# Performance work log

Measured on AMD Instinct MI355X. Metric: run time of the kernel, lower is better.

## Reference

```python
import jax, jax.numpy as jnp
import numpy as np

H = 8  # n_heads


def _accumulate(carry, args):
    # carry: csum [B,H,l,d], norm [B,H,l], prev_mx [B,H,l]  (l=L//H, d=D//H)
    csum, norm, prev_mx = carry
    Qs_t, K_t, V_t, c_mx = args
    revert = jnp.exp(prev_mx - c_mx)               # rescale old accum to new max
    add = jnp.exp(K_t - c_mx)                      # exp(k_t) stabilized
    norm = norm * revert + add                     # [B,H,l]
    csum = csum * revert[..., None] + add[..., None] * V_t[:, :, None, :]  # [B,H,l,d]
    y = jnp.einsum('bhl,bhld->bhd', Qs_t / norm, csum)
    return (csum, norm, c_mx), y


def setup_inputs() -> dict:
    key = jax.random.key(0)
    B, T, D, L = 4, 2048, 1024, 512
    k0, k1, k2, k3, k4 = jax.random.split(key, 5)
    X = jax.random.normal(k0, (B, T, D), jnp.float32)
    # lecun_normal: std = 1/sqrt(fan_in)
    Wk = jax.random.normal(k1, (D, L), jnp.float32) * (1.0 / np.sqrt(D))
    Wq = jax.random.normal(k2, (D, L), jnp.float32) * (1.0 / np.sqrt(D))
    Wv = jax.random.normal(k3, (D, D), jnp.float32) * (1.0 / np.sqrt(D))
    o_proj = jax.random.normal(k4, (D, D), jnp.float32) * (1.0 / np.sqrt(D))
    return {"X": X, "Wk": Wk, "Wq": Wq, "Wv": Wv, "o_proj": o_proj, "train": False}


def reference(X, Wk, Wq, Wv, o_proj, train):
    # train=False -> dropouts are deterministic identities
    B, T, D = X.shape
    L = Wk.shape[1]
    V = jnp.einsum('dm,btd->tbm', Wv, X).reshape(T, B, H, D // H)
    Q = jnp.einsum('dl,btd->tbl', Wq, X).reshape(T, B, H, L // H)
    K = jnp.einsum('dl,btd->tbl', Wk, X).reshape(T, B, H, L // H)
    maxi = jax.lax.stop_gradient(jax.lax.cummax(K, axis=0))  # running max over time
    Qs = jax.nn.softmax(Q, axis=-1)
    init = (jnp.zeros((B, H, L // H, D // H), X.dtype),
            jnp.zeros((B, H, L // H), X.dtype),
            K[0])
    _, y = jax.lax.scan(_accumulate, init, (Qs, K, V, maxi), unroll=8)
    y = y.transpose(1, 0, 2, 3).reshape(B, T, D)
    return y @ o_proj
```

## Files before the change

### kernel.cpp

```cpp
#include <hip/hip_runtime.h>
#include <hip/hip_bf16.h>


typedef __attribute__((ext_vector_type(8))) short bf16x8;
typedef __attribute__((ext_vector_type(4))) float f32x4;

__device__ inline ushort f2bf(float f) {
    unsigned u = __float_as_uint(f);
    unsigned r = (u + 0x7fff + ((u >> 16) & 1)) >> 16;
    return (ushort)r;
}
__device__ inline float bf2f(ushort h) { return __uint_as_float(((unsigned)h) << 16); }

__device__ inline void gload_lds16(const ushort* g, ushort* l) {
    __builtin_amdgcn_global_load_lds((const __attribute__((address_space(1))) void*)g,
                                     (__attribute__((address_space(3))) void*)l, 16, 0, 0);
}

__global__ __launch_bounds__(256) void prep_inputs_kernel(const float* __restrict__ X,
                                                          const float* __restrict__ Wq,
                                                          const float* __restrict__ Wk,
                                                          const float* __restrict__ Wv,
                                                          const float* __restrict__ Wo,
                                                          ushort* __restrict__ Xb,
                                                          ushort* __restrict__ WqkT,
                                                          ushort* __restrict__ WvT,
                                                          ushort* __restrict__ WoT) {
    if (blockIdx.x < 8192) {
        int i = blockIdx.x * 1024 + threadIdx.x * 4;
        float4 v = *(const float4*)(X + i);
        ushort4 o = {f2bf(v.x), f2bf(v.y), f2bf(v.z), f2bf(v.w)};
        *(ushort4*)(Xb + i) = o;
        return;
    }
    __shared__ float s[32][33];
    int t = blockIdx.x - 8192;
    const float* W; ushort* WT; int N, tile, rowoff;
    if (t < 512)       { W = Wq; WT = WqkT; N = 512;  tile = t;        rowoff = 0; }
    else if (t < 1024) { W = Wk; WT = WqkT; N = 512;  tile = t - 512;  rowoff = 512; }
    else if (t < 2048) { W = Wv; WT = WvT;  N = 1024; tile = t - 1024; rowoff = 0; }
    else               { W = Wo; WT = WoT;  N = 1024; tile = t - 2048; rowoff = 0; }
    int tilesX = N >> 5;
    int n0 = (tile % tilesX) * 32, k0 = (tile / tilesX) * 32;
    int tx = threadIdx.x & 31, ty0 = threadIdx.x >> 5;
#pragma unroll
    for (int r = 0; r < 4; ++r) {
        int row = ty0 + r * 8;
        s[row][tx] = W[(size_t)(k0 + row) * N + n0 + tx];
    }
    __syncthreads();
#pragma unroll
    for (int r = 0; r < 4; ++r) {
        int row = ty0 + r * 8;
        WT[(size_t)(rowoff + n0 + row) * 1024 + k0 + tx] = f2bf(s[tx][row]);
    }
}

__global__ __launch_bounds__(256) void qk_gemm(const ushort* __restrict__ A,
                                               const ushort* __restrict__ BT,
                                               ushort* __restrict__ Qb,
                                               ushort* __restrict__ Kbp,
                                               float* __restrict__ mbuf,
                                               float* __restrict__ sbuf) {
    __shared__ __align__(16) ushort As[128 * 32];
    __shared__ __align__(16) ushort Bs[128 * 32];
    __shared__ float sredM[2][128];
    __shared__ float sredS[2][128];
    const int K = 1024;
    const int tid = threadIdx.x;
    const int w = tid >> 6, lane = tid & 63;
    const int quad = lane >> 4, l15 = lane & 15;
    const int m0 = blockIdx.y * 128, n0 = blockIdx.x * 128;
    const int wm = (w & 1) * 64, wn = (w >> 1) * 64;
    f32x4 acc[4][4] = {};
    const int r0 = tid >> 2, kc = (tid & 3) * 8;
    const int r1 = 64 + r0;
    const ushort* Arow0 = A + (size_t)(m0 + r0) * K + kc;
    const ushort* Arow1 = A + (size_t)(m0 + r1) * K + kc;
    const ushort* Brow0 = BT + (size_t)(n0 + r0) * K + kc;
    const ushort* Brow1 = BT + (size_t)(n0 + r1) * K + kc;
    ushort* AsW0 = As + (w * 64) * 8;
    ushort* AsW1 = As + (256 + w * 64) * 8;
    ushort* BsW0 = Bs + (w * 64) * 8;
    ushort* BsW1 = Bs + (256 + w * 64) * 8;
    const ushort* afp = As + (wm + l15) * 32 + quad * 8;
    const ushort* bfp = Bs + (wn + l15) * 32 + quad * 8;
    for (int k0 = 0; k0 < K; k0 += 32) {
        gload_lds16(Arow0 + k0, AsW0);
        gload_lds16(Arow1 + k0, AsW1);
        gload_lds16(Brow0 + k0, BsW0);
        gload_lds16(Brow1 + k0, BsW1);
        __syncthreads();
        bf16x8 af[4], bf[4];
#pragma unroll
        for (int i = 0; i < 4; ++i) {
            af[i] = *(const bf16x8*)(afp + i * 16 * 32);
            bf[i] = *(const bf16x8*)(bfp + i * 16 * 32);
        }
#pragma unroll
        for (int i = 0; i < 4; ++i)
#pragma unroll
            for (int j = 0; j < 4; ++j)
                acc[i][j] = __builtin_amdgcn_mfma_f32_16x16x32_bf16(af[i], bf[j], acc[i][j], 0, 0, 0);
        __syncthreads();
    }
    const int crow = m0 + wm + quad * 4;
    const int ccol = n0 + wn + l15;
    if (n0 < 512) {
#pragma unroll
        for (int i = 0; i < 4; ++i)
#pragma unroll
            for (int r = 0; r < 4; ++r) {
                float x0 = acc[i][0][r], x1 = acc[i][1][r];
                float x2 = acc[i][2][r], x3 = acc[i][3][r];
                float m = fmaxf(fmaxf(x0, x1), fmaxf(x2, x3));
#pragma unroll
                for (int off = 1; off < 16; off <<= 1) m = fmaxf(m, __shfl_xor(m, off));
                float e0 = __expf(x0 - m), e1 = __expf(x1 - m);
                float e2 = __expf(x2 - m), e3 = __expf(x3 - m);
                float s = (e0 + e1) + (e2 + e3);
#pragma unroll
                for (int off = 1; off < 16; off <<= 1) s += __shfl_xor(s, off);
                float rs = 1.0f / s;
                acc[i][0][r] = e0 * rs; acc[i][1][r] = e1 * rs;
                acc[i][2][r] = e2 * rs; acc[i][3][r] = e3 * rs;
            }
#pragma unroll
        for (int i = 0; i < 4; ++i)
#pragma unroll
            for (int j = 0; j < 4; ++j) {
                f32x4 v = acc[i][j];
#pragma unroll
                for (int r = 0; r < 4; ++r)
                    Qb[(size_t)(crow + i * 16 + r) * 512 + ccol + j * 16] = f2bf(v[r]);
            }
    } else {
        int b = blockIdx.y >> 4, c = blockIdx.y & 15;
        float mj[4];
#pragma unroll
        for (int j = 0; j < 4; ++j) {
            float m = -1e30f;
#pragma unroll
            for (int i = 0; i < 4; ++i)
#pragma unroll
                for (int r = 0; r < 4; ++r) m = fmaxf(m, acc[i][j][r]);
            m = fmaxf(m, __shfl_xor(m, 16));
            m = fmaxf(m, __shfl_xor(m, 32));
            mj[j] = m;
        }
        if (quad == 0)
#pragma unroll
            for (int j = 0; j < 4; ++j) sredM[w & 1][(w >> 1) * 64 + j * 16 + l15] = mj[j];
        __syncthreads();
#pragma unroll
        for (int j = 0; j < 4; ++j) {
            int ci = (w >> 1) * 64 + j * 16 + l15;
            float M = fmaxf(sredM[0][ci], sredM[1][ci]);
            float s = 0.f;
#pragma unroll
            for (int i = 0; i < 4; ++i)
#pragma unroll
                for (int r = 0; r < 4; ++r) s += __expf(acc[i][j][r] - M);
            s += __shfl_xor(s, 16);
            s += __shfl_xor(s, 32);
            mj[j] = s;
        }
        if (quad == 0)
#pragma unroll
            for (int j = 0; j < 4; ++j) sredS[w & 1][(w >> 1) * 64 + j * 16 + l15] = mj[j];
        __syncthreads();
        if (tid < 128) {
            int Kcol = (n0 - 512) + tid;
            int h = Kcol >> 6, l = Kcol & 63;
            int idx = (((b * 8 + h) * 16 + c)) * 64 + l;
            mbuf[idx] = fmaxf(sredM[0][tid], sredM[1][tid]);
            sbuf[idx] = sredS[0][tid] + sredS[1][tid];
        }
#pragma unroll
        for (int i = 0; i < 4; ++i)
#pragma unroll
            for (int j = 0; j < 4; ++j) {
                f32x4 v = acc[i][j];
#pragma unroll
                for (int r = 0; r < 4; ++r)
                    Kbp[(size_t)(crow + i * 16 + r) * 512 + (ccol - 512) + j * 16] = f2bf(v[r]);
            }
    }
}

__global__ __launch_bounds__(256) void vt_gemm(const ushort* __restrict__ A,
                                               const ushort* __restrict__ BT,
                                               ushort* __restrict__ VT) {
    __shared__ __align__(16) ushort As[128 * 32];
    __shared__ __align__(16) ushort Bs[128 * 32];
    __shared__ __align__(16) ushort Ts[128 * 136];
    const int K = 1024;
    const int tid = threadIdx.x;
    const int w = tid >> 6, lane = tid & 63;
    const int quad = lane >> 4, l15 = lane & 15;
    const int m0 = blockIdx.y * 128, n0 = blockIdx.x * 128;
    const int wm = (w & 1) * 64, wn = (w >> 1) * 64;
    f32x4 acc[4][4] = {};
    const int r0 = tid >> 2, kc = (tid & 3) * 8;
    const int r1 = 64 + r0;
    const ushort* Arow0 = A + (size_t)(m0 + r0) * K + kc;
    const ushort* Arow1 = A + (size_t)(m0 + r1) * K + kc;
    const ushort* Brow0 = BT + (size_t)(n0 + r0) * K + kc;
    const ushort* Brow1 = BT + (size_t)(n0 + r1) * K + kc;
    ushort* AsW0 = As + (w * 64) * 8;
    ushort* AsW1 = As + (256 + w * 64) * 8;
    ushort* BsW0 = Bs + (w * 64) * 8;
    ushort* BsW1 = Bs + (256 + w * 64) * 8;
    const ushort* afp = As + (wm + l15) * 32 + quad * 8;
    const ushort* bfp = Bs + (wn + l15) * 32 + quad * 8;
    for (int k0 = 0; k0 < K; k0 += 32) {
        gload_lds16(Arow0 + k0, AsW0);
        gload_lds16(Arow1 + k0, AsW1);
        gload_lds16(Brow0 + k0, BsW0);
        gload_lds16(Brow1 + k0, BsW1);
        __syncthreads();
        bf16x8 af[4], bf[4];
#pragma unroll
        for (int i = 0; i < 4; ++i) {
            af[i] = *(const bf16x8*)(afp + i * 16 * 32);
            bf[i] = *(const bf16x8*)(bfp + i * 16 * 32);
        }
#pragma unroll
        for (int i = 0; i < 4; ++i)
#pragma unroll
            for (int j = 0; j < 4; ++j)
                acc[i][j] = __builtin_amdgcn_mfma_f32_16x16x32_bf16(af[i], bf[j], acc[i][j], 0, 0, 0);
        __syncthreads();
    }
#pragma unroll
    for (int i = 0; i < 4; ++i)
#pragma unroll
        for (int j = 0; j < 4; ++j) {
            f32x4 v = acc[i][j];
            int d = wn + j * 16 + l15;
            int t = wm + i * 16 + quad * 4;
            ushort4 o = {f2bf(v[0]), f2bf(v[1]), f2bf(v[2]), f2bf(v[3])};
            *(ushort4*)(Ts + d * 136 + t) = o;
        }
    __syncthreads();
    int b = m0 >> 11, tloc = m0 & 2047, h = n0 >> 7;
    ushort* base = VT + ((size_t)(b * 8 + h) * 128) * 2048 + tloc;
    int kk = tid & 7;
#pragma unroll
    for (int p = 0; p < 4; ++p) {
        int dd = p * 32 + (tid >> 3);
        const uint4* src = (const uint4*)(Ts + dd * 136 + kk * 16);
        uint4* dst = (uint4*)(base + (size_t)dd * 2048 + kk * 16);
        dst[0] = src[0];
        dst[1] = src[1];
    }
}

__global__ __launch_bounds__(256) void prep_scanP_kernel(const ushort* __restrict__ Kbuf,
                                                         const ushort* __restrict__ Qs,
                                                         const float* __restrict__ mbuf,
                                                         const float* __restrict__ sbuf,
                                                         ushort* __restrict__ abuf,
                                                         ushort* __restrict__ aTbuf,
                                                         ushort* __restrict__ Pbuf) {
    __shared__ float red[4][64];
    int blk = blockIdx.x, bh = blk >> 4, c = blk & 15;
    int b = bh >> 3, h = bh & 7;
    int tg = threadIdx.x >> 6, l = threadIdx.x & 63;
    float mc[16];
#pragma unroll
    for (int cc = 0; cc < 16; ++cc) mc[cc] = mbuf[(bh * 16 + cc) * 64 + l];
    float M = -1e30f;
#pragma unroll
    for (int cc = 0; cc < 16; ++cc) M = fmaxf(M, mc[cc]);
    float A0 = 0.f;
    for (int cc = 0; cc < c; ++cc) A0 += sbuf[(bh * 16 + cc) * 64 + l] * __expf(mc[cc] - M);
    const ushort* kp = Kbuf + ((size_t)(b * 2048 + c * 128 + tg * 32)) * 512 + h * 64 + l;
    const ushort* qp = Qs + ((size_t)(b * 2048 + c * 128 + tg * 32)) * 512 + h * 64 + l;
    float a[32];
#pragma unroll
    for (int i = 0; i < 32; ++i) a[i] = __expf(bf2f(kp[(size_t)i * 512]) - M);
    float part = 0.f;
#pragma unroll
    for (int i = 0; i < 32; ++i) part += a[i];
    red[tg][l] = part;
    __syncthreads();
    float A = A0;
    for (int g = 0; g < 4; ++g) {
        float v = red[g][l];
        A += (g < tg) ? v : 0.f;
    }
    ushort* ap = abuf + ((size_t)(bh * 2048 + c * 128 + tg * 32)) * 64 + l;
    ushort* pp = Pbuf + ((size_t)(bh * 2048 + c * 128 + tg * 32)) * 64 + l;
    ushort atmp[32];
#pragma unroll
    for (int i = 0; i < 32; ++i) {
        A += a[i];
        ushort ab16 = f2bf(a[i]);
        ap[(size_t)i * 64] = ab16;
        atmp[i] = ab16;
        pp[(size_t)i * 64] = f2bf(bf2f(qp[(size_t)i * 512]) / A);
    }
    ushort* atp = aTbuf + ((size_t)bh * 64 + l) * 2048 + c * 128 + tg * 32;
#pragma unroll
    for (int v = 0; v < 4; ++v) *(uint4*)(atp + v * 8) = *(const uint4*)(atmp + v * 8);
}

__global__ __launch_bounds__(256) void chunk_sums_mfma(const ushort* __restrict__ aT,
                                                       const ushort* __restrict__ VT,
                                                       float* __restrict__ S) {
    int blk = blockIdx.x, bh = blk >> 4, c = blk & 15;
    int w = threadIdx.x >> 6, lane = threadIdx.x & 63;
    int quad = lane >> 4, l15 = lane & 15;
    const ushort* vtb = VT + (size_t)bh * 128 * 2048 + c * 128;
    const ushort* atb = aT + (size_t)bh * 64 * 2048 + c * 128;
    f32x4 acc[2][4] = {};
#pragma unroll
    for (int ks = 0; ks < 4; ++ks) {
        bf16x8 af[2];
#pragma unroll
        for (int mi = 0; mi < 2; ++mi)
            af[mi] = *(const bf16x8*)(vtb + (size_t)(w * 32 + mi * 16 + l15) * 2048 + ks * 32 + quad * 8);
#pragma unroll
        for (int nj = 0; nj < 4; ++nj) {
            bf16x8 bfr = *(const bf16x8*)(atb + (size_t)(nj * 16 + l15) * 2048 + ks * 32 + quad * 8);
#pragma unroll
            for (int mi = 0; mi < 2; ++mi)
                acc[mi][nj] = __builtin_amdgcn_mfma_f32_16x16x32_bf16(af[mi], bfr, acc[mi][nj], 0, 0, 0);
        }
    }
    float* sp = S + (size_t)blk * 8192;
#pragma unroll
    for (int mi = 0; mi < 2; ++mi)
#pragma unroll
        for (int nj = 0; nj < 4; ++nj) {
            f32x4 v = acc[mi][nj];
#pragma unroll
            for (int r = 0; r < 4; ++r)
                sp[(w * 32 + mi * 16 + quad * 4 + r) * 64 + nj * 16 + l15] = v[r];
        }
}

__global__ __launch_bounds__(256) void chunk_prefix_kernel(float* __restrict__ Sbuf) {
    int gid = blockIdx.x * 256 + threadIdx.x;
    int l = gid & 63, d = (gid >> 6) & 127, bh = gid >> 13;
    float run = 0.f;
    for (int c = 0; c < 16; ++c) {
        size_t idx = (size_t)(bh * 16 + c) * 8192 + d * 64 + l;
        float t = Sbuf[idx];
        Sbuf[idx] = run;
        run += t;
    }
}

__global__ __launch_bounds__(256) void chunk_out_mfma(const ushort* __restrict__ ab,
                                                      const ushort* __restrict__ Pb,
                                                      const ushort* __restrict__ VT,
                                                      const float* __restrict__ S,
                                                      ushort* __restrict__ Yb) {
    __shared__ __align__(16) ushort Gs[128 * 136];
    int blk = blockIdx.x, bh = blk >> 4, c = blk & 15;
    int b = bh >> 3, h = bh & 7;
    int w = threadIdx.x >> 6, lane = threadIdx.x & 63;
    int quad = lane >> 4, l15 = lane & 15;
    const ushort* Pc = Pb + (size_t)(bh * 2048 + c * 128) * 64;
    const ushort* Ac = ab + (size_t)(bh * 2048 + c * 128) * 64;
    f32x4 g[8][2] = {};
#pragma unroll
    for (int ks = 0; ks < 2; ++ks) {
        bf16x8 bfr[2];
#pragma unroll
        for (int ni = 0; ni < 2; ++ni)
            bfr[ni] = *(const bf16x8*)(Pc + (w * 32 + ni * 16 + l15) * 64 + ks * 32 + quad * 8);
#pragma unroll
        for (int ms = 0; ms < 8; ++ms) {
            bf16x8 af = *(const bf16x8*)(Ac + (ms * 16 + l15) * 64 + ks * 32 + quad * 8);
#pragma unroll
            for (int ni = 0; ni < 2; ++ni)
                g[ms][ni] = __builtin_amdgcn_mfma_f32_16x16x32_bf16(af, bfr[ni], g[ms][ni], 0, 0, 0);
        }
    }
#pragma unroll
    for (int ms = 0; ms < 8; ++ms)
#pragma unroll
        for (int ni = 0; ni < 2; ++ni) {
            int iL = w * 32 + ni * 16 + l15;
            int sBase = ms * 16 + quad * 4;
            f32x4 v = g[ms][ni];
            ushort4 o;
            o.x = (sBase + 0 <= iL) ? f2bf(v[0]) : (ushort)0;
            o.y = (sBase + 1 <= iL) ? f2bf(v[1]) : (ushort)0;
            o.z = (sBase + 2 <= iL) ? f2bf(v[2]) : (ushort)0;
            o.w = (sBase + 3 <= iL) ? f2bf(v[3]) : (ushort)0;
            *(ushort4*)(Gs + iL * 136 + sBase) = o;
        }
    __syncthreads();
    const ushort* vtb = VT + (size_t)bh * 128 * 2048 + c * 128;
    const float* sp = S + (size_t)blk * 8192;
    f32x4 y[2][8] = {};
#pragma unroll
    for (int ks = 0; ks < 4; ++ks) {
        bf16x8 af[2];
#pragma unroll
        for (int mi = 0; mi < 2; ++mi)
            af[mi] = *(const bf16x8*)(Gs + (w * 32 + mi * 16 + l15) * 136 + ks * 32 + quad * 8);
#pragma unroll
        for (int nj = 0; nj < 8; ++nj) {
            bf16x8 bfr = *(const bf16x8*)(vtb + (size_t)(nj * 16 + l15) * 2048 + ks * 32 + quad * 8);
#pragma unroll
            for (int mi = 0; mi < 2; ++mi)
                y[mi][nj] = __builtin_amdgcn_mfma_f32_16x16x32_bf16(af[mi], bfr, y[mi][nj], 0, 0, 0);
        }
    }
#pragma unroll
    for (int ks = 0; ks < 2; ++ks) {
        bf16x8 af[2];
#pragma unroll
        for (int mi = 0; mi < 2; ++mi)
            af[mi] = *(const bf16x8*)(Pc + (w * 32 + mi * 16 + l15) * 64 + ks * 32 + quad * 8);
#pragma unroll
        for (int nj = 0; nj < 8; ++nj) {
            const float* s8 = sp + (nj * 16 + l15) * 64 + ks * 32 + quad * 8;
            float4 f0 = *(const float4*)s8;
            float4 f1 = *(const float4*)(s8 + 4);
            bf16x8 bfr;
            bfr[0] = (short)f2bf(f0.x); bfr[1] = (short)f2bf(f0.y);
            bfr[2] = (short)f2bf(f0.z); bfr[3] = (short)f2bf(f0.w);
            bfr[4] = (short)f2bf(f1.x); bfr[5] = (short)f2bf(f1.y);
            bfr[6] = (short)f2bf(f1.z); bfr[7] = (short)f2bf(f1.w);
#pragma unroll
            for (int mi = 0; mi < 2; ++mi)
                y[mi][nj] = __builtin_amdgcn_mfma_f32_16x16x32_bf16(af[mi], bfr, y[mi][nj], 0, 0, 0);
        }
    }
    ushort* yout = Yb + ((size_t)(b * 2048 + c * 128)) * 1024 + h * 128;
#pragma unroll
    for (int mi = 0; mi < 2; ++mi)
#pragma unroll
        for (int nj = 0; nj < 8; ++nj) {
            f32x4 v = y[mi][nj];
#pragma unroll
            for (int r = 0; r < 4; ++r) {
                int iL = w * 32 + mi * 16 + quad * 4 + r;
                yout[(size_t)iL * 1024 + nj * 16 + l15] = f2bf(v[r]);
            }
        }
}

__global__ __launch_bounds__(256) void mfma_gemm(const ushort* __restrict__ A,
                                                 const ushort* __restrict__ BT,
                                                 float* __restrict__ Cf,
                                                 int M, int N, int K) {
    __shared__ __align__(16) ushort As[128 * 32];
    __shared__ __align__(16) ushort Bs[128 * 32];
    const int tid = threadIdx.x;
    const int w = tid >> 6, lane = tid & 63;
    const int quad = lane >> 4, l15 = lane & 15;
    const int m0 = blockIdx.y * 128, n0 = blockIdx.x * 128;
    const int wm = (w & 1) * 64, wn = (w >> 1) * 64;
    f32x4 acc[4][4] = {};
    const int r0 = tid >> 2, kc = (tid & 3) * 8;
    const int r1 = 64 + r0;
    const ushort* Arow0 = A + (size_t)(m0 + r0) * K + kc;
    const ushort* Arow1 = A + (size_t)(m0 + r1) * K + kc;
    const ushort* Brow0 = BT + (size_t)(n0 + r0) * K + kc;
    const ushort* Brow1 = BT + (size_t)(n0 + r1) * K + kc;
    ushort* AsW0 = As + (w * 64) * 8;
    ushort* AsW1 = As + (256 + w * 64) * 8;
    ushort* BsW0 = Bs + (w * 64) * 8;
    ushort* BsW1 = Bs + (256 + w * 64) * 8;
    const ushort* afp = As + (wm + l15) * 32 + quad * 8;
    const ushort* bfp = Bs + (wn + l15) * 32 + quad * 8;
    for (int k0 = 0; k0 < K; k0 += 32) {
        gload_lds16(Arow0 + k0, AsW0);
        gload_lds16(Arow1 + k0, AsW1);
        gload_lds16(Brow0 + k0, BsW0);
        gload_lds16(Brow1 + k0, BsW1);
        __syncthreads();
        bf16x8 af[4], bf[4];
#pragma unroll
        for (int i = 0; i < 4; ++i) {
            af[i] = *(const bf16x8*)(afp + i * 16 * 32);
            bf[i] = *(const bf16x8*)(bfp + i * 16 * 32);
        }
#pragma unroll
        for (int i = 0; i < 4; ++i)
#pragma unroll
            for (int j = 0; j < 4; ++j)
                acc[i][j] = __builtin_amdgcn_mfma_f32_16x16x32_bf16(af[i], bf[j], acc[i][j], 0, 0, 0);
        __syncthreads();
    }
    const int crow = m0 + wm + quad * 4;
    const int ccol = n0 + wn + l15;
#pragma unroll
    for (int i = 0; i < 4; ++i)
#pragma unroll
        for (int j = 0; j < 4; ++j) {
            f32x4 v = acc[i][j];
#pragma unroll
            for (int r = 0; r < 4; ++r)
                Cf[(size_t)(crow + i * 16 + r) * N + ccol + j * 16] = v[r];
        }
}

extern "C" void kernel_launch(void* const* d_in, const int* in_sizes, int n_in,
                              void* d_out, int out_size, void* d_ws, size_t ws_size,
                              hipStream_t stream) {
    const float* X  = (const float*)d_in[0];
    const float* Wk = (const float*)d_in[1];
    const float* Wq = (const float*)d_in[2];
    const float* Wv = (const float*)d_in[3];
    const float* Wo = (const float*)d_in[4];
    float* ws = (float*)d_ws;
    ushort* Xb   = (ushort*)ws;
    ushort* Qs   = (ushort*)(ws + 4194304);
    ushort* Kb   = (ushort*)(ws + 6291456);
    ushort* VT   = (ushort*)(ws + 8388608);
    ushort* ab   = (ushort*)(ws + 12582912);
    ushort* aT   = (ushort*)(ws + 14680064);
    ushort* Pb   = (ushort*)(ws + 16777216);
    float*  Sb   = ws + 18874368;
    ushort* WqkT = (ushort*)(ws + 22020096);
    ushort* WvT  = (ushort*)(ws + 22544384);
    ushort* WoT  = (ushort*)(ws + 23068672);
    ushort* Yb = Xb;
    float* out = (float*)d_out;
    float* mbuf = out;
    float* sbuf = out + 32768;

    dim3 blk(256);
    prep_inputs_kernel<<<11264, blk, 0, stream>>>(X, Wq, Wk, Wv, Wo, Xb, WqkT, WvT, WoT);
    qk_gemm<<<dim3(8, 64), blk, 0, stream>>>(Xb, WqkT, Qs, Kb, mbuf, sbuf);
    vt_gemm<<<dim3(8, 64), blk, 0, stream>>>(Xb, WvT, VT);
    prep_scanP_kernel<<<512, blk, 0, stream>>>(Kb, Qs, mbuf, sbuf, ab, aT, Pb);
    chunk_sums_mfma<<<512, blk, 0, stream>>>(aT, VT, Sb);
    chunk_prefix_kernel<<<1024, blk, 0, stream>>>(Sb);
    chunk_out_mfma<<<512, blk, 0, stream>>>(ab, Pb, VT, Sb, Yb);
    mfma_gemm<<<dim3(8, 64), blk, 0, stream>>>(Yb, WoT, out, 8192, 1024, 1024);
}
```

Baseline: 243.5 us.

## Fuse QK and V GEMMs, fuse scan prep with chunk sums, store chunk state in bf16

Merges the QK and V projection GEMMs into a single launch with a 16x64 grid, where blocks pick their weight matrix by blockIdx.x. Also merges prep_scanP with chunk_sums so the transposed decay coefficients stay in LDS rather than round-tripping through a global aT buffer. Chunk state S is now stored in bf16 instead of fp32, which halves its traffic and drops the float-to-bf16 conversion in chunk_out. In exchange, the prefix sum now accumulates values rounded to bf16, and the fused GEMM carries the larger shared-memory footprint for all blocks, which may reduce occupancy.

```diff
diff --git a/kernel.cpp b/kernel.cpp
--- a/kernel.cpp
+++ b/kernel.cpp
@@ -56,21 +56,27 @@
     }
 }
 
-__global__ __launch_bounds__(256) void qk_gemm(const ushort* __restrict__ A,
-                                               const ushort* __restrict__ BT,
-                                               ushort* __restrict__ Qb,
-                                               ushort* __restrict__ Kbp,
-                                               float* __restrict__ mbuf,
-                                               float* __restrict__ sbuf) {
+__global__ __launch_bounds__(256) void qkv_gemm(const ushort* __restrict__ A,
+                                                const ushort* __restrict__ WqkT,
+                                                const ushort* __restrict__ WvT,
+                                                ushort* __restrict__ Qb,
+                                                ushort* __restrict__ Kbp,
+                                                ushort* __restrict__ VT,
+                                                float* __restrict__ mbuf,
+                                                float* __restrict__ sbuf) {
     __shared__ __align__(16) ushort As[128 * 32];
     __shared__ __align__(16) ushort Bs[128 * 32];
+    __shared__ __align__(16) ushort Ts[128 * 136];
     __shared__ float sredM[2][128];
     __shared__ float sredS[2][128];
     const int K = 1024;
     const int tid = threadIdx.x;
     const int w = tid >> 6, lane = tid & 63;
     const int quad = lane >> 4, l15 = lane & 15;
-    const int m0 = blockIdx.y * 128, n0 = blockIdx.x * 128;
+    const bool isQK = blockIdx.x < 8;
+    const int nx = isQK ? blockIdx.x : (blockIdx.x - 8);
+    const ushort* BT = isQK ? WqkT : WvT;
+    const int m0 = blockIdx.y * 128, n0 = nx * 128;
     const int wm = (w & 1) * 64, wn = (w >> 1) * 64;
     f32x4 acc[4][4] = {};
     const int r0 = tid >> 2, kc = (tid & 3) * 8;
@@ -106,6 +112,31 @@
     }
     const int crow = m0 + wm + quad * 4;
     const int ccol = n0 + wn + l15;
+    if (!isQK) {
+#pragma unroll
+        for (int i = 0; i < 4; ++i)
+#pragma unroll
+            for (int j = 0; j < 4; ++j) {
+                f32x4 v = acc[i][j];
+                int d = wn + j * 16 + l15;
+                int t = wm + i * 16 + quad * 4;
+                ushort4 o = {f2bf(v[0]), f2bf(v[1]), f2bf(v[2]), f2bf(v[3])};
+                *(ushort4*)(Ts + d * 136 + t) = o;
+            }
+        __syncthreads();
+        int b = m0 >> 11, tloc = m0 & 2047, h = n0 >> 7;
+        ushort* base = VT + ((size_t)(b * 8 + h) * 128) * 2048 + tloc;
+        int kk = tid & 7;
+#pragma unroll
+        for (int p = 0; p < 4; ++p) {
+            int dd = p * 32 + (tid >> 3);
+            const uint4* src = (const uint4*)(Ts + dd * 136 + kk * 16);
+            uint4* dst = (uint4*)(base + (size_t)dd * 2048 + kk * 16);
+            dst[0] = src[0];
+            dst[1] = src[1];
+        }
+        return;
+    }
     if (n0 < 512) {
 #pragma unroll
         for (int i = 0; i < 4; ++i)
@@ -188,82 +219,16 @@
     }
 }
 
-__global__ __launch_bounds__(256) void vt_gemm(const ushort* __restrict__ A,
-                                               const ushort* __restrict__ BT,
-                                               ushort* __restrict__ VT) {
-    __shared__ __align__(16) ushort As[128 * 32];
-    __shared__ __align__(16) ushort Bs[128 * 32];
-    __shared__ __align__(16) ushort Ts[128 * 136];
-    const int K = 1024;
-    const int tid = threadIdx.x;
-    const int w = tid >> 6, lane = tid & 63;
-    const int quad = lane >> 4, l15 = lane & 15;
-    const int m0 = blockIdx.y * 128, n0 = blockIdx.x * 128;
-    const int wm = (w & 1) * 64, wn = (w >> 1) * 64;
-    f32x4 acc[4][4] = {};
-    const int r0 = tid >> 2, kc = (tid & 3) * 8;
-    const int r1 = 64 + r0;
-    const ushort* Arow0 = A + (size_t)(m0 + r0) * K + kc;
-    const ushort* Arow1 = A + (size_t)(m0 + r1) * K + kc;
-    const ushort* Brow0 = BT + (size_t)(n0 + r0) * K + kc;
-    const ushort* Brow1 = BT + (size_t)(n0 + r1) * K + kc;
-    ushort* AsW0 = As + (w * 64) * 8;
-    ushort* AsW1 = As + (256 + w * 64) * 8;
-    ushort* BsW0 = Bs + (w * 64) * 8;
-    ushort* BsW1 = Bs + (256 + w * 64) * 8;
-    const ushort* afp = As + (wm + l15) * 32 + quad * 8;
-    const ushort* bfp = Bs + (wn + l15) * 32 + quad * 8;
-    for (int k0 = 0; k0 < K; k0 += 32) {
-        gload_lds16(Arow0 + k0, AsW0);
-        gload_lds16(Arow1 + k0, AsW1);
-        gload_lds16(Brow0 + k0, BsW0);
-        gload_lds16(Brow1 + k0, BsW1);
-        __syncthreads();
-        bf16x8 af[4], bf[4];
-#pragma unroll
-        for (int i = 0; i < 4; ++i) {
-            af[i] = *(const bf16x8*)(afp + i * 16 * 32);
-            bf[i] = *(const bf16x8*)(bfp + i * 16 * 32);
-        }
-#pragma unroll
-        for (int i = 0; i < 4; ++i)
-#pragma unroll
-            for (int j = 0; j < 4; ++j)
-                acc[i][j] = __builtin_amdgcn_mfma_f32_16x16x32_bf16(af[i], bf[j], acc[i][j], 0, 0, 0);
-        __syncthreads();
-    }
-#pragma unroll
-    for (int i = 0; i < 4; ++i)
-#pragma unroll
-        for (int j = 0; j < 4; ++j) {
-            f32x4 v = acc[i][j];
-            int d = wn + j * 16 + l15;
-            int t = wm + i * 16 + quad * 4;
-            ushort4 o = {f2bf(v[0]), f2bf(v[1]), f2bf(v[2]), f2bf(v[3])};
-            *(ushort4*)(Ts + d * 136 + t) = o;
-        }
-    __syncthreads();
-    int b = m0 >> 11, tloc = m0 & 2047, h = n0 >> 7;
-    ushort* base = VT + ((size_t)(b * 8 + h) * 128) * 2048 + tloc;
-    int kk = tid & 7;
-#pragma unroll
-    for (int p = 0; p < 4; ++p) {
-        int dd = p * 32 + (tid >> 3);
-        const uint4* src = (const uint4*)(Ts + dd * 136 + kk * 16);
-        uint4* dst = (uint4*)(base + (size_t)dd * 2048 + kk * 16);
-        dst[0] = src[0];
-        dst[1] = src[1];
-    }
-}
-
-__global__ __launch_bounds__(256) void prep_scanP_kernel(const ushort* __restrict__ Kbuf,
-                                                         const ushort* __restrict__ Qs,
-                                                         const float* __restrict__ mbuf,
-                                                         const float* __restrict__ sbuf,
-                                                         ushort* __restrict__ abuf,
-                                                         ushort* __restrict__ aTbuf,
-                                                         ushort* __restrict__ Pbuf) {
+__global__ __launch_bounds__(256) void prep_scan_sums_kernel(const ushort* __restrict__ Kbuf,
+                                                             const ushort* __restrict__ Qs,
+                                                             const float* __restrict__ mbuf,
+                                                             const float* __restrict__ sbuf,
+                                                             const ushort* __restrict__ VT,
+                                                             ushort* __restrict__ abuf,
+                                                             ushort* __restrict__ Pbuf,
+                                                             ushort* __restrict__ Sb) {
     __shared__ float red[4][64];
+    __shared__ __align__(16) ushort aS[64 * 136];
     int blk = blockIdx.x, bh = blk >> 4, c = blk & 15;
     int b = bh >> 3, h = bh & 7;
     int tg = threadIdx.x >> 6, l = threadIdx.x & 63;
@@ -301,19 +266,13 @@
         atmp[i] = ab16;
         pp[(size_t)i * 64] = f2bf(bf2f(qp[(size_t)i * 512]) / A);
     }
-    ushort* atp = aTbuf + ((size_t)bh * 64 + l) * 2048 + c * 128 + tg * 32;
-#pragma unroll
-    for (int v = 0; v < 4; ++v) *(uint4*)(atp + v * 8) = *(const uint4*)(atmp + v * 8);
-}
-
-__global__ __launch_bounds__(256) void chunk_sums_mfma(const ushort* __restrict__ aT,
-                                                       const ushort* __restrict__ VT,
-                                                       float* __restrict__ S) {
-    int blk = blockIdx.x, bh = blk >> 4, c = blk & 15;
+    ushort* asp = aS + l * 136 + tg * 32;
+#pragma unroll
+    for (int v = 0; v < 4; ++v) *(uint4*)(asp + v * 8) = *(const uint4*)(atmp + v * 8);
+    __syncthreads();
     int w = threadIdx.x >> 6, lane = threadIdx.x & 63;
     int quad = lane >> 4, l15 = lane & 15;
     const ushort* vtb = VT + (size_t)bh * 128 * 2048 + c * 128;
-    const ushort* atb = aT + (size_t)bh * 64 * 2048 + c * 128;
     f32x4 acc[2][4] = {};
 #pragma unroll
     for (int ks = 0; ks < 4; ++ks) {
@@ -323,13 +282,13 @@
             af[mi] = *(const bf16x8*)(vtb + (size_t)(w * 32 + mi * 16 + l15) * 2048 + ks * 32 + quad * 8);
 #pragma unroll
         for (int nj = 0; nj < 4; ++nj) {
-            bf16x8 bfr = *(const bf16x8*)(atb + (size_t)(nj * 16 + l15) * 2048 + ks * 32 + quad * 8);
+            bf16x8 bfr = *(const bf16x8*)(aS + (nj * 16 + l15) * 136 + ks * 32 + quad * 8);
 #pragma unroll
             for (int mi = 0; mi < 2; ++mi)
                 acc[mi][nj] = __builtin_amdgcn_mfma_f32_16x16x32_bf16(af[mi], bfr, acc[mi][nj], 0, 0, 0);
         }
     }
-    float* sp = S + (size_t)blk * 8192;
+    ushort* sp = Sb + (size_t)blk * 8192;
 #pragma unroll
     for (int mi = 0; mi < 2; ++mi)
 #pragma unroll
@@ -337,18 +296,18 @@
             f32x4 v = acc[mi][nj];
 #pragma unroll
             for (int r = 0; r < 4; ++r)
-                sp[(w * 32 + mi * 16 + quad * 4 + r) * 64 + nj * 16 + l15] = v[r];
-        }
-}
-
-__global__ __launch_bounds__(256) void chunk_prefix_kernel(float* __restrict__ Sbuf) {
+                sp[(w * 32 + mi * 16 + quad * 4 + r) * 64 + nj * 16 + l15] = f2bf(v[r]);
+        }
+}
+
+__global__ __launch_bounds__(256) void chunk_prefix_kernel(ushort* __restrict__ Sbuf) {
     int gid = blockIdx.x * 256 + threadIdx.x;
     int l = gid & 63, d = (gid >> 6) & 127, bh = gid >> 13;
     float run = 0.f;
     for (int c = 0; c < 16; ++c) {
         size_t idx = (size_t)(bh * 16 + c) * 8192 + d * 64 + l;
-        float t = Sbuf[idx];
-        Sbuf[idx] = run;
+        float t = bf2f(Sbuf[idx]);
+        Sbuf[idx] = f2bf(run);
         run += t;
     }
 }
@@ -356,7 +315,7 @@
 __global__ __launch_bounds__(256) void chunk_out_mfma(const ushort* __restrict__ ab,
                                                       const ushort* __restrict__ Pb,
                                                       const ushort* __restrict__ VT,
-                                                      const float* __restrict__ S,
+                                                      const ushort* __restrict__ S,
                                                       ushort* __restrict__ Yb) {
     __shared__ __align__(16) ushort Gs[128 * 136];
     int blk = blockIdx.x, bh = blk >> 4, c = blk & 15;
@@ -396,7 +355,7 @@
         }
     __syncthreads();
     const ushort* vtb = VT + (size_t)bh * 128 * 2048 + c * 128;
-    const float* sp = S + (size_t)blk * 8192;
+    const ushort* sp = S + (size_t)blk * 8192;
     f32x4 y[2][8] = {};
 #pragma unroll
     for (int ks = 0; ks < 4; ++ks) {
@@ -420,14 +379,7 @@
             af[mi] = *(const bf16x8*)(Pc + (w * 32 + mi * 16 + l15) * 64 + ks * 32 + quad * 8);
 #pragma unroll
         for (int nj = 0; nj < 8; ++nj) {
-            const float* s8 = sp + (nj * 16 + l15) * 64 + ks * 32 + quad * 8;
-            float4 f0 = *(const float4*)s8;
-            float4 f1 = *(const float4*)(s8 + 4);
-            bf16x8 bfr;
-            bfr[0] = (short)f2bf(f0.x); bfr[1] = (short)f2bf(f0.y);
-            bfr[2] = (short)f2bf(f0.z); bfr[3] = (short)f2bf(f0.w);
-            bfr[4] = (short)f2bf(f1.x); bfr[5] = (short)f2bf(f1.y);
-            bfr[6] = (short)f2bf(f1.z); bfr[7] = (short)f2bf(f1.w);
+            bf16x8 bfr = *(const bf16x8*)(sp + (nj * 16 + l15) * 64 + ks * 32 + quad * 8);
 #pragma unroll
             for (int mi = 0; mi < 2; ++mi)
                 y[mi][nj] = __builtin_amdgcn_mfma_f32_16x16x32_bf16(af[mi], bfr, y[mi][nj], 0, 0, 0);
@@ -517,12 +469,11 @@
     ushort* Kb   = (ushort*)(ws + 6291456);
     ushort* VT   = (ushort*)(ws + 8388608);
     ushort* ab   = (ushort*)(ws + 12582912);
-    ushort* aT   = (ushort*)(ws + 14680064);
-    ushort* Pb   = (ushort*)(ws + 16777216);
-    float*  Sb   = ws + 18874368;
-    ushort* WqkT = (ushort*)(ws + 22020096);
-    ushort* WvT  = (ushort*)(ws + 22544384);
-    ushort* WoT  = (ushort*)(ws + 23068672);
+    ushort* Pb   = (ushort*)(ws + 14680064);
+    ushort* Sb   = (ushort*)(ws + 16777216);
+    ushort* WqkT = (ushort*)(ws + 18874368);
+    ushort* WvT  = (ushort*)(ws + 19398656);
+    ushort* WoT  = (ushort*)(ws + 19922944);
     ushort* Yb = Xb;
     float* out = (float*)d_out;
     float* mbuf = out;
@@ -530,10 +481,8 @@
 
     dim3 blk(256);
     prep_inputs_kernel<<<11264, blk, 0, stream>>>(X, Wq, Wk, Wv, Wo, Xb, WqkT, WvT, WoT);
-    qk_gemm<<<dim3(8, 64), blk, 0, stream>>>(Xb, WqkT, Qs, Kb, mbuf, sbuf);
-    vt_gemm<<<dim3(8, 64), blk, 0, stream>>>(Xb, WvT, VT);
-    prep_scanP_kernel<<<512, blk, 0, stream>>>(Kb, Qs, mbuf, sbuf, ab, aT, Pb);
-    chunk_sums_mfma<<<512, blk, 0, stream>>>(aT, VT, Sb);
+    qkv_gemm<<<dim3(16, 64), blk, 0, stream>>>(Xb, WqkT, WvT, Qs, Kb, VT, mbuf, sbuf);
+    prep_scan_sums_kernel<<<512, blk, 0, stream>>>(Kb, Qs, mbuf, sbuf, VT, ab, Pb, Sb);
     chunk_prefix_kernel<<<1024, blk, 0, stream>>>(Sb);
     chunk_out_mfma<<<512, blk, 0, stream>>>(ab, Pb, VT, Sb, Yb);
     mfma_gemm<<<dim3(8, 64), blk, 0, stream>>>(Yb, WoT, out, 8192, 1024, 1024);
```

After: 224.6 us. 7.8% less time.
